# Kernel optimization log

Hardware: AMD Instinct MI355X
Metric: run time of the kernel (lower is better)

Reference implementation:

```python
import jax, jax.numpy as jnp
import numpy as np

C_IN = 64
C_QK = C_IN // 8  # 8
B, H, W = 8, 64, 64


def setup_inputs() -> dict:
    key = jax.random.key(0)
    ks = jax.random.split(key, 8)
    s_in = 1.0 / np.sqrt(C_IN)
    return {
        "x": jax.random.normal(ks[0], (B, C_IN, H, W), dtype=jnp.float32),
        "Wf": jax.random.normal(ks[1], (C_QK, C_IN), dtype=jnp.float32) * s_in,
        "bf": jax.random.normal(ks[2], (C_QK,), dtype=jnp.float32) * 0.01,
        "Wg": jax.random.normal(ks[3], (C_QK, C_IN), dtype=jnp.float32) * s_in,
        "bg": jax.random.normal(ks[4], (C_QK,), dtype=jnp.float32) * 0.01,
        "Wh": jax.random.normal(ks[5], (C_IN, C_IN), dtype=jnp.float32) * s_in,
        "bh": jax.random.normal(ks[6], (C_IN,), dtype=jnp.float32) * 0.01,
        "gamma": jax.random.normal(ks[7], (1,), dtype=jnp.float32) * 0.1,
    }


def reference(x, Wf, bf, Wg, bg, Wh, bh, gamma):
    Bn, C, Hn, Wn = x.shape
    N = Hn * Wn
    xf = x.reshape(Bn, C, N)  # (B, C, HW)
    # 1x1 convs == per-pixel linear projections
    fx = jnp.einsum('bcn,oc->bno', xf, Wf) + bf            # (B, HW, C/8)  (permuted query)
    gx = jnp.einsum('bcn,oc->bon', xf, Wg) + bg[:, None]   # (B, C/8, HW)
    hx = jnp.einsum('bcn,oc->bon', xf, Wh) + bh[:, None]   # (B, C,  HW)
    s_mtx = jnp.einsum('bno,bom->bnm', fx, gx)             # (B, HW, HW)
    attention = jax.nn.softmax(s_mtx, axis=-2)             # softmax over dim=-2 (rows)
    o = jnp.einsum('bcn,bnm->bcm', hx, attention)          # (B, C, HW)
    return x + gamma * o.reshape(Bn, C, Hn, Wn)
```

## Files before the change

### kernel.cpp

```cpp
#include <hip/hip_runtime.h>
#include <hip/hip_bf16.h>
#include <math.h>

#define CIN 64
#define CQK 8
#define BATCH 8
#define NPOS 4096
#define TN 256
#define NT (NPOS / TN)

typedef __attribute__((ext_vector_type(8))) short s16x8;
typedef __attribute__((ext_vector_type(4))) float f32x4;
typedef __attribute__((ext_vector_type(16))) float f32x16;

#define Z16 {0,0,0,0,0,0,0,0,0,0,0,0,0,0,0,0}

#define SCH_BIAS 1065353216.0f

__device__ inline unsigned cvt_pk_bf16(float lo, float hi) {
    unsigned r;
    asm("v_cvt_pk_bf16_f32 %0, %1, %2" : "=v"(r) : "v"(lo), "v"(hi));
    return r;
}
__device__ inline float sch_exp(float y) {
    return __builtin_bit_cast(float, (int)y);
}

__global__ __launch_bounds__(256) void proj_kernel(
    const float* __restrict__ x,
    const float* __restrict__ Wf, const float* __restrict__ bf,
    const float* __restrict__ Wg, const float* __restrict__ bg,
    const float* __restrict__ Wh, const float* __restrict__ bh,
    unsigned short* __restrict__ Kp, unsigned short* __restrict__ Qp,
    unsigned short* __restrict__ Vimg)
{
    __shared__ float xs[CIN * 34];
    __shared__ float bss[80];

    const int tid = threadIdx.x;
    const int b   = blockIdx.y;
    const int n0  = blockIdx.x * 32;

    if (tid < 80)
        bss[tid] = (tid < 8) ? bf[tid] : (tid < 16) ? bg[tid - 8] : bh[tid - 16];

    {
        const int c   = tid >> 2;
        const int seg = tid & 3;
        const float* src = x + ((size_t)(b * CIN + c)) * NPOS + n0 + seg * 8;
        float* dst = xs + c * 34 + seg * 8;
#pragma unroll
        for (int k = 0; k < 2; ++k) {
            const float4 v = *(const float4*)(src + k * 4);
            *(float2*)(dst + k * 4)     = make_float2(v.x, v.y);
            *(float2*)(dst + k * 4 + 2) = make_float2(v.z, v.w);
        }
    }

    const int l    = tid & 63;
    const int w    = tid >> 6;
    const int ng   = w >> 1;
    const int role = w & 1;
    const int lm   = l & 15;
    const int h    = l >> 4;

    auto wfrag = [&](const float* Wrow) -> s16x8 {
        const float4 a  = *(const float4*)(Wrow);
        const float4 bq = *(const float4*)(Wrow + 4);
        union { unsigned u[4]; s16x8 v; } r;
        r.u[0] = cvt_pk_bf16(a.x, a.y);
        r.u[1] = cvt_pk_bf16(a.z, a.w);
        r.u[2] = cvt_pk_bf16(bq.x, bq.y);
        r.u[3] = cvt_pk_bf16(bq.z, bq.w);
        return r.v;
    };

    s16x8 wkq0 = {0,0,0,0,0,0,0,0}, wkq1 = {0,0,0,0,0,0,0,0};
    if (role == 0) {
        const float* kqrow = (lm < 8) ? (Wf + lm * CIN) : (Wg + (lm - 8) * CIN);
        wkq0 = wfrag(kqrow + h * 8);
        wkq1 = wfrag(kqrow + h * 8 + 32);
    }
    s16x8 wv0[2], wv1[2];
#pragma unroll
    for (int vt = 0; vt < 2; ++vt) {
        const float* vr = Wh + ((role * 2 + vt) * 16 + lm) * CIN + h * 8;
        wv0[vt] = wfrag(vr);
        wv1[vt] = wfrag(vr + 32);
    }

    __syncthreads();

    union { unsigned u[4]; s16x8 v; } xf0, xf1;
#pragma unroll
    for (int e2 = 0; e2 < 4; ++e2) {
        const int c = h * 8 + e2 * 2;
        xf0.u[e2] = cvt_pk_bf16(xs[c * 34 + ng * 16 + lm],
                                xs[(c + 1) * 34 + ng * 16 + lm]);
        xf1.u[e2] = cvt_pk_bf16(xs[(c + 32) * 34 + ng * 16 + lm],
                                xs[(c + 33) * 34 + ng * 16 + lm]);
    }

    const f32x4 z = {0.f, 0.f, 0.f, 0.f};
    f32x4 va[2];
#pragma unroll
    for (int vt = 0; vt < 2; ++vt) {
        va[vt] = __builtin_amdgcn_mfma_f32_16x16x32_bf16(xf0.v, wv0[vt], z, 0, 0, 0);
        va[vt] = __builtin_amdgcn_mfma_f32_16x16x32_bf16(xf1.v, wv1[vt], va[vt], 0, 0, 0);
    }

    const float QSCALE = 1.44269504088896f * 8388608.0f;

    if (role == 0) {
        f32x4 kq = __builtin_amdgcn_mfma_f32_16x16x32_bf16(wkq0, xf0.v, z, 0, 0, 0);
        kq = __builtin_amdgcn_mfma_f32_16x16x32_bf16(wkq1, xf1.v, kq, 0, 0, 0);
        const int n = n0 + ng * 16 + lm;
        float v0 = kq[0] + bss[h * 4 + 0];
        float v1 = kq[1] + bss[h * 4 + 1];
        float v2 = kq[2] + bss[h * 4 + 2];
        float v3 = kq[3] + bss[h * 4 + 3];
        if (h >= 2) { v0 *= QSCALE; v1 *= QSCALE; v2 *= QSCALE; v3 *= QSCALE; }
        uint2 pk;
        pk.x = cvt_pk_bf16(v0, v1);
        pk.y = cvt_pk_bf16(v2, v3);
        unsigned short* dstq =
            (h < 2 ? Kp : Qp) + ((size_t)(b * NPOS + n)) * CQK + (h & 1) * 4;
        *(uint2*)dstq = pk;
    }

    {
        const int t128 = n0 >> 7;
        const int sub  = (n0 & 127) >> 5;
        unsigned short* dstB =
            Vimg + ((size_t)(b * 32 + t128)) * 8192 + (size_t)sub * 2048;
        const int jj   = (h & 1) * 2 + ng;
        const int half = h >> 1;
#pragma unroll
        for (int vt = 0; vt < 2; ++vt) {
            const int C = (role * 2 + vt) * 16 + lm;
            const float bb = bss[16 + C];
            uint2 pk;
            pk.x = cvt_pk_bf16(va[vt][0] + bb, va[vt][1] + bb);
            pk.y = cvt_pk_bf16(va[vt][2] + bb, va[vt][3] + bb);
            const int p = ((jj & 1) * 2 + (C >> 5)) * 64 + (jj >> 1) * 32 + (C & 31);
            *(uint2*)(dstB + p * 8 + half * 4) = pk;
        }
    }
}

__global__ __launch_bounds__(256, 2) void attn_kernel(
    const unsigned short* __restrict__ Kp, const unsigned short* __restrict__ Qp,
    const unsigned short* __restrict__ Vimg, const float* __restrict__ x,
    const float* __restrict__ gamma, float* __restrict__ out)
{
    __shared__ __align__(16) float smem[4 * 64 * 36 + 256];
    float* reg = smem;
    float* rsl = smem + 4 * 64 * 36;

    const int tid = threadIdx.x;
    const int l   = tid & 63;
    const int w   = tid >> 6;
    const int lc  = l & 31;
    const int h   = l >> 5;
    const int id  = blockIdx.x;
    const int b   = id & 7;
    const int m0  = (id >> 3) * 64;

    const unsigned short* Kbat = Kp + (size_t)b * NPOS * CQK;
    const char* Vbat = (const char*)(Vimg + (size_t)b * NPOS * CIN);

    s16x8 qf0 = {0,0,0,0,0,0,0,0}, qf1 = {0,0,0,0,0,0,0,0};
    if (h == 0) {
        qf0 = *(const s16x8*)(Qp + ((size_t)(b * NPOS + m0 + lc)) * CQK);
        qf1 = *(const s16x8*)(Qp + ((size_t)(b * NPOS + m0 + 32 + lc)) * CQK);
    }

    f32x16 acc00 = Z16, acc01 = Z16, acc10 = Z16, acc11 = Z16;
    float rsum0 = 0.f, rsum1 = 0.f;
    const f32x16 bias16 = {SCH_BIAS, SCH_BIAS, SCH_BIAS, SCH_BIAS,
                           SCH_BIAS, SCH_BIAS, SCH_BIAS, SCH_BIAS,
                           SCH_BIAS, SCH_BIAS, SCH_BIAS, SCH_BIAS,
                           SCH_BIAS, SCH_BIAS, SCH_BIAS, SCH_BIAS};

    s16x8 vfA[8], vfB[8], kaA[2], kaB[2];

    auto loadG0 = [&](s16x8* vf, s16x8* ka, int t) {
        const char* kb = (const char*)(Kbat + ((size_t)(t * TN + w * 64 + lc)) * CQK);
        ka[0] = *(const s16x8*)kb;
        const char* base = Vbat + (size_t)t * 32768 + w * 8192 + l * 16;
#pragma unroll
        for (int c = 0; c < 4; ++c)
            vf[c] = *(const s16x8*)(base + c * 1024);
    };
    auto loadG1 = [&](s16x8* vf, s16x8* ka, int t) {
        const char* kb = (const char*)(Kbat + ((size_t)(t * TN + w * 64 + lc)) * CQK);
        ka[1] = *(const s16x8*)(kb + 32 * 16);
        const char* base = Vbat + (size_t)t * 32768 + w * 8192 + l * 16;
#pragma unroll
        for (int c = 4; c < 8; ++c)
            vf[c] = *(const s16x8*)(base + c * 1024);
    };

    auto half_step = [&](const s16x8& kah, const s16x8* vfh) {
        f32x16 sc0 = __builtin_amdgcn_mfma_f32_32x32x16_bf16(kah, qf0, bias16, 0, 0, 0);
        f32x16 sc1 = __builtin_amdgcn_mfma_f32_32x32x16_bf16(kah, qf1, bias16, 0, 0, 0);
        float p0[16], p1[16];
#pragma unroll
        for (int i = 0; i < 16; ++i) {
            p0[i] = sch_exp(sc0[i]);
            p1[i] = sch_exp(sc1[i]);
        }
        union { unsigned u[4]; s16x8 v; } A1, A2, B1, B2;
#pragma unroll
        for (int i = 0; i < 4; ++i) {
            A1.u[i] = cvt_pk_bf16(p0[2 * i],     p0[2 * i + 1]);
            A2.u[i] = cvt_pk_bf16(p0[8 + 2 * i], p0[9 + 2 * i]);
            B1.u[i] = cvt_pk_bf16(p1[2 * i],     p1[2 * i + 1]);
            B2.u[i] = cvt_pk_bf16(p1[8 + 2 * i], p1[9 + 2 * i]);
        }
        rsum0 += (((p0[0] + p0[1]) + (p0[2] + p0[3])) +
                  ((p0[4] + p0[5]) + (p0[6] + p0[7]))) +
                 (((p0[8] + p0[9]) + (p0[10] + p0[11])) +
                  ((p0[12] + p0[13]) + (p0[14] + p0[15])));
        rsum1 += (((p1[0] + p1[1]) + (p1[2] + p1[3])) +
                  ((p1[4] + p1[5]) + (p1[6] + p1[7]))) +
                 (((p1[8] + p1[9]) + (p1[10] + p1[11])) +
                  ((p1[12] + p1[13]) + (p1[14] + p1[15])));
        acc00 = __builtin_amdgcn_mfma_f32_32x32x16_bf16(A1.v, vfh[0], acc00, 0, 0, 0);
        acc01 = __builtin_amdgcn_mfma_f32_32x32x16_bf16(A1.v, vfh[1], acc01, 0, 0, 0);
        acc10 = __builtin_amdgcn_mfma_f32_32x32x16_bf16(B1.v, vfh[0], acc10, 0, 0, 0);
        acc11 = __builtin_amdgcn_mfma_f32_32x32x16_bf16(B1.v, vfh[1], acc11, 0, 0, 0);
        acc00 = __builtin_amdgcn_mfma_f32_32x32x16_bf16(A2.v, vfh[2], acc00, 0, 0, 0);
        acc01 = __builtin_amdgcn_mfma_f32_32x32x16_bf16(A2.v, vfh[3], acc01, 0, 0, 0);
        acc10 = __builtin_amdgcn_mfma_f32_32x32x16_bf16(B2.v, vfh[2], acc10, 0, 0, 0);
        acc11 = __builtin_amdgcn_mfma_f32_32x32x16_bf16(B2.v, vfh[3], acc11, 0, 0, 0);
    };

    auto slot = [&](s16x8* vf, s16x8* ka, int t, int drain, int pf) {
        if (drain) asm volatile("s_waitcnt vmcnt(0)"  ::: "memory");
        else       asm volatile("s_waitcnt vmcnt(10)" ::: "memory");
        __builtin_amdgcn_s_setprio(1);
        half_step(ka[0], vf);
        __builtin_amdgcn_s_setprio(0);
        if (pf) loadG0(vf, ka, t + 2);
        __builtin_amdgcn_s_setprio(1);
        half_step(ka[1], vf + 4);
        __builtin_amdgcn_s_setprio(0);
        if (pf) loadG1(vf, ka, t + 2);
    };

    loadG0(vfA, kaA, 0); loadG1(vfA, kaA, 0);
    loadG0(vfB, kaB, 1); loadG1(vfB, kaB, 1);

#pragma unroll 1
    for (int i = 0; i < 7; ++i) {
        slot(vfA, kaA, 2 * i,     0, 1);
        slot(vfB, kaB, 2 * i + 1, 0, 1);
    }
    slot(vfA, kaA, 14, 0, 0);
    slot(vfB, kaB, 15, 1, 0);

    rsum0 += __shfl_xor(rsum0, 32, 64);
    rsum1 += __shfl_xor(rsum1, 32, 64);
    if (h == 0) {
        rsl[w * 64 + lc]      = rsum0;
        rsl[w * 64 + 32 + lc] = rsum1;
    }

    const float gm = gamma[0];
    auto epi = [&](const f32x16& a0, const f32x16& a1, int mOff) {
#pragma unroll
        for (int rq = 0; rq < 4; ++rq) {
            const int mb = 8 * rq + 4 * h;
            const f32x4 q0 = {a0[4 * rq], a0[4 * rq + 1], a0[4 * rq + 2], a0[4 * rq + 3]};
            const f32x4 q1 = {a1[4 * rq], a1[4 * rq + 1], a1[4 * rq + 2], a1[4 * rq + 3]};
            *(f32x4*)(reg + w * 2304 + lc * 36 + mb)        = q0;
            *(f32x4*)(reg + w * 2304 + (32 + lc) * 36 + mb) = q1;
        }
        __syncthreads();
        const int c  = tid >> 2;
        const int mq = tid & 3;
        const size_t base = ((size_t)(b * CIN + c)) * NPOS + m0 + mOff + mq * 8;
#pragma unroll
        for (int q4 = 0; q4 < 2; ++q4) {
            const float4 xv = *(const float4*)(x + base + q4 * 4);
            float4 o;
#pragma unroll
            for (int i = 0; i < 4; ++i) {
                const int ml = mq * 8 + q4 * 4 + i;
                const float rsum = (rsl[mOff + ml] + rsl[64 + mOff + ml]) +
                                   (rsl[128 + mOff + ml] + rsl[192 + mOff + ml]);
                const int oi = c * 36 + ml;
                const float os = (reg[oi] + reg[2304 + oi]) + (reg[4608 + oi] + reg[6912 + oi]);
                ((float*)&o)[i] = ((const float*)&xv)[i] + gm * os / rsum;
            }
            *(float4*)(out + base + q4 * 4) = o;
        }
        __syncthreads();
    };
    epi(acc00, acc01, 0);
    epi(acc10, acc11, 32);
}

extern "C" void kernel_launch(void* const* d_in, const int* in_sizes, int n_in,
                              void* d_out, int out_size, void* d_ws, size_t ws_size,
                              hipStream_t stream) {
    const float* x     = (const float*)d_in[0];
    const float* Wf    = (const float*)d_in[1];
    const float* bf    = (const float*)d_in[2];
    const float* Wg    = (const float*)d_in[3];
    const float* bg    = (const float*)d_in[4];
    const float* Wh    = (const float*)d_in[5];
    const float* bh    = (const float*)d_in[6];
    const float* gamma = (const float*)d_in[7];
    float* out = (float*)d_out;

    unsigned short* Kp   = (unsigned short*)d_ws;
    unsigned short* Qp   = Kp + (size_t)BATCH * NPOS * CQK;
    unsigned short* Vimg = Qp + (size_t)BATCH * NPOS * CQK;

    dim3 pgrid(NPOS / 32, BATCH);
    proj_kernel<<<pgrid, 256, 0, stream>>>(x, Wf, bf, Wg, bg, Wh, bh, Kp, Qp, Vimg);

    attn_kernel<<<dim3(BATCH * NPOS / 64), 256, 0, stream>>>(Kp, Qp, Vimg, x, gamma, out);
}
```

Baseline: 37.08 us.

## Stagger per-block key tile order and wait on half-tile loads separately

After: 37.71 us. Within noise of the previous version (+1.7%).

```diff
diff --git a/kernel.cpp b/kernel.cpp
--- a/kernel.cpp
+++ b/kernel.cpp
@@ -165,6 +165,7 @@
     const int id  = blockIdx.x;
     const int b   = id & 7;
     const int m0  = (id >> 3) * 64;
+    const int phase = ((id >> 3) + (id >> 7)) & (NT - 1);
 
     const unsigned short* Kbat = Kp + (size_t)b * NPOS * CQK;
     const char* Vbat = (const char*)(Vimg + (size_t)b * NPOS * CIN);
@@ -184,18 +185,18 @@
 
     s16x8 vfA[8], vfB[8], kaA[2], kaB[2];
 
-    auto loadG0 = [&](s16x8* vf, s16x8* ka, int t) {
-        const char* kb = (const char*)(Kbat + ((size_t)(t * TN + w * 64 + lc)) * CQK);
+    auto loadG0 = [&](s16x8* vf, s16x8* ka, int tp) {
+        const char* kb = (const char*)(Kbat + ((size_t)(tp * TN + w * 64 + lc)) * CQK);
         ka[0] = *(const s16x8*)kb;
-        const char* base = Vbat + (size_t)t * 32768 + w * 8192 + l * 16;
+        const char* base = Vbat + (size_t)tp * 32768 + w * 8192 + l * 16;
 #pragma unroll
         for (int c = 0; c < 4; ++c)
             vf[c] = *(const s16x8*)(base + c * 1024);
     };
-    auto loadG1 = [&](s16x8* vf, s16x8* ka, int t) {
-        const char* kb = (const char*)(Kbat + ((size_t)(t * TN + w * 64 + lc)) * CQK);
+    auto loadG1 = [&](s16x8* vf, s16x8* ka, int tp) {
+        const char* kb = (const char*)(Kbat + ((size_t)(tp * TN + w * 64 + lc)) * CQK);
         ka[1] = *(const s16x8*)(kb + 32 * 16);
-        const char* base = Vbat + (size_t)t * 32768 + w * 8192 + l * 16;
+        const char* base = Vbat + (size_t)tp * 32768 + w * 8192 + l * 16;
 #pragma unroll
         for (int c = 4; c < 8; ++c)
             vf[c] = *(const s16x8*)(base + c * 1024);
@@ -236,29 +237,33 @@
         acc11 = __builtin_amdgcn_mfma_f32_32x32x16_bf16(B2.v, vfh[3], acc11, 0, 0, 0);
     };
 
-    auto slot = [&](s16x8* vf, s16x8* ka, int t, int drain, int pf) {
-        if (drain) asm volatile("s_waitcnt vmcnt(0)"  ::: "memory");
-        else       asm volatile("s_waitcnt vmcnt(10)" ::: "memory");
+    auto slot = [&](s16x8* vf, s16x8* ka, int t, int mode) {
+        const int tp = (t + 2 + phase) & (NT - 1);
+        if (mode == 2) asm volatile("s_waitcnt vmcnt(5)"  ::: "memory");
+        else           asm volatile("s_waitcnt vmcnt(15)" ::: "memory");
         __builtin_amdgcn_s_setprio(1);
         half_step(ka[0], vf);
         __builtin_amdgcn_s_setprio(0);
-        if (pf) loadG0(vf, ka, t + 2);
+        if (mode == 0) loadG0(vf, ka, tp);
+        if (mode == 0)      asm volatile("s_waitcnt vmcnt(15)" ::: "memory");
+        else if (mode == 1) asm volatile("s_waitcnt vmcnt(10)" ::: "memory");
+        else                asm volatile("s_waitcnt vmcnt(0)"  ::: "memory");
         __builtin_amdgcn_s_setprio(1);
         half_step(ka[1], vf + 4);
         __builtin_amdgcn_s_setprio(0);
-        if (pf) loadG1(vf, ka, t + 2);
-    };
-
-    loadG0(vfA, kaA, 0); loadG1(vfA, kaA, 0);
-    loadG0(vfB, kaB, 1); loadG1(vfB, kaB, 1);
+        if (mode == 0) loadG1(vf, ka, tp);
+    };
+
+    loadG0(vfA, kaA, phase);              loadG1(vfA, kaA, phase);
+    loadG0(vfB, kaB, (1 + phase) & (NT - 1)); loadG1(vfB, kaB, (1 + phase) & (NT - 1));
 
 #pragma unroll 1
     for (int i = 0; i < 7; ++i) {
-        slot(vfA, kaA, 2 * i,     0, 1);
-        slot(vfB, kaB, 2 * i + 1, 0, 1);
-    }
-    slot(vfA, kaA, 14, 0, 0);
-    slot(vfB, kaB, 15, 1, 0);
+        slot(vfA, kaA, 2 * i,     0);
+        slot(vfB, kaB, 2 * i + 1, 0);
+    }
+    slot(vfA, kaA, 14, 1);
+    slot(vfB, kaB, 15, 2);
 
     rsum0 += __shfl_xor(rsum0, 32, 64);
     rsum1 += __shfl_xor(rsum1, 32, 64);
```
